# Optimization experiments

Hardware: AMD Instinct MI355X
Metric: run time of the kernel (lower is better)

## Reference

```python
import jax, jax.numpy as jnp
import numpy as np
from jax import lax

T_PN = (1, 1, 2, 2, 2, 4, 4, 4, 4, 4)
V_PN = (1, 2, 3, 4, 5, 6, 8, 10, 13, 16)
N_CODES = 16384
EMBED_DIM = 64
QRESI = 0.5           # abs(quant_resi), quant_resi = -0.5 -> ks=3 conv
K_SHARED = 4          # share_quant_resi


def _pool_mat(in_len, out_len):
    """torch F.interpolate(mode='area') == adaptive average pooling."""
    M = np.zeros((out_len, in_len), np.float32)
    for i in range(out_len):
        s = (i * in_len) // out_len
        e = -((-(i + 1) * in_len) // out_len)  # ceil((i+1)*in/out)
        M[i, s:e] = 1.0 / (e - s)
    return jnp.asarray(M)


def _lin_mat(in_len, out_len):
    """torch linear/trilinear upsample (align_corners=False) per-axis weights."""
    M = np.zeros((out_len, in_len), np.float32)
    if in_len == 1:
        M[:, 0] = 1.0
        return jnp.asarray(M)
    scale = in_len / out_len
    for i in range(out_len):
        src = max((i + 0.5) * scale - 0.5, 0.0)
        i0 = min(int(np.floor(src)), in_len - 1)
        i1 = min(i0 + 1, in_len - 1)
        w = src - i0
        M[i, i0] += 1.0 - w
        M[i, i1] += w
    return jnp.asarray(M)


def _resi_idx(si, n_scales):
    # ResConvAfterUpsampleList.__getitem__ : nearest tick to si/(n_scales-1)
    ticks = np.linspace(1.0 / 3 / K_SHARED, 1.0 - 1.0 / 3 / K_SHARED, K_SHARED)
    return int(np.argmin(np.abs(ticks - si / max(1, n_scales - 1))))


def _conv3d(x, w, b):
    y = lax.conv_general_dilated(x, w, (1, 1, 1), 'SAME',
                                 dimension_numbers=('NCDHW', 'OIDHW', 'NCDHW'))
    return y + b[None, :, None, None, None]


def setup_inputs() -> dict:
    key = jax.random.key(0)
    k1, k2, k3, k4 = jax.random.split(key, 4)
    z = jax.random.normal(k1, (8, EMBED_DIM, 4, 16, 16), dtype=jnp.float32)
    embeddings = jax.random.normal(k2, (N_CODES, EMBED_DIM), dtype=jnp.float32)
    Wq = jax.random.normal(k3, (K_SHARED, EMBED_DIM, EMBED_DIM, 3, 3, 3), dtype=jnp.float32) * 0.02
    bq = jax.random.normal(k4, (K_SHARED, EMBED_DIM), dtype=jnp.float32) * 0.02
    return {"z": z, "embeddings": embeddings, "Wq": Wq, "bq": bq}


def reference(z, embeddings, Wq, bq):
    B, C, T, H, W = z.shape
    S = len(V_PN)
    z_sg = lax.stop_gradient(z)
    accu = jnp.zeros_like(z)
    commit = jnp.asarray(0.0, z.dtype)
    ms_idx = []
    e_sq = jnp.sum(embeddings * embeddings, axis=1)  # [n_codes]
    for si, (tpn, pn) in enumerate(zip(T_PN, V_PN)):
        tpn = min(tpn, T)
        # rest uses detached accu (accu_h.data in torch)
        rest = z_sg - lax.stop_gradient(accu)
        if si != S - 1:
            rest = jnp.einsum('bcthw,ut,vh,xw->bcuvx', rest,
                              _pool_mat(T, tpn), _pool_mat(H, pn), _pool_mat(W, pn))
        zNC = rest.transpose(0, 2, 3, 4, 1).reshape(-1, C)  # [N, C]
        # ||z||^2 + ||e||^2 - 2 z.e  (the addmm)
        d = jnp.sum(zNC * zNC, axis=1, keepdims=True) + e_sq - 2.0 * (zNC @ embeddings.T)
        idx = jnp.argmin(d, axis=1).reshape(rest.shape[0], *rest.shape[2:])  # [B,t,p,p]
        ms_idx.append(idx)
        h = embeddings[idx].transpose(0, 4, 1, 2, 3)  # [B,C,t,p,p]
        if h.shape[2:] != (T, H, W):
            h = jnp.einsum('bcthw,ut,vh,xw->bcuvx', h,
                           _lin_mat(tpn, T), _lin_mat(pn, H), _lin_mat(pn, W))
        qi = _resi_idx(si, S)
        h = h * (1.0 - QRESI) + _conv3d(h, Wq[qi], bq[qi]) * QRESI
        accu = accu + h
        commit = commit + 0.25 * jnp.mean((accu - z_sg) ** 2)
    commit = commit / S
    emb_st = lax.stop_gradient(accu - z) + z  # straight-through
    # eval-mode stats come from the LAST scale's indices (loop-variable leak in torch)
    last = ms_idx[-1].reshape(-1)
    probs = jnp.bincount(last, length=N_CODES).astype(z.dtype) / last.shape[0]
    perplexity = jnp.exp(-jnp.sum(probs * jnp.log(probs + 1e-10)))
    usage = probs  # counts/total == calculate_batch_codebook_usage_percentage
    avg_usage = jnp.sum(usage > 1.0 / N_CODES).astype(z.dtype) / N_CODES
    return (emb_st, commit, perplexity, avg_usage, usage) + tuple(ms_idx)
```

## Files before the change

### kernel.cpp

```cpp
#include <hip/hip_runtime.h>
#include <math.h>


#define NCODES 16384
#define NELEM  524288
#define NSP    8192

#define RCH    8
#define RCODES (NCODES / RCH)

#define WS_ACCU   0ul
#define WS_HUP    4194304ul
#define WS_REST64 8388608ul
#define WS_PACC   8388608ul
#define WS_PART   12582912ul
#define WS_ZCL    16777216ul
#define WS_EHF    18874368ul
#define WS_ELF    20971520ul
#define WS_ESQ    23068672ul
#define WS_TWT    23134208ul
#define WS_IDX    24903680ul
#define WS_CNT    24936448ul
#define WS_FLAGL  25001984ul
#define WS_FLAGC  25034752ul
#define WS_SSE    25034816ul
#define WS_ENT    25034824ul
#define WS_USED   25034832ul
#define WS_RHF    25034848ul
#define WS_RLF    26083424ul

typedef __attribute__((ext_vector_type(8))) short short8;
typedef __attribute__((ext_vector_type(4))) float floatx4;

struct PBest { double d; int idx; int pad; };

__device__ __forceinline__ void gl2lds16(const void* g, void* l) {
  __builtin_amdgcn_global_load_lds(
      (const __attribute__((address_space(1))) unsigned int*)g,
      (__attribute__((address_space(3))) unsigned int*)l, 16, 0, 0);
}

__device__ inline short bf16rne(float f, float* hi) {
  unsigned u = __float_as_uint(f);
  unsigned r = (u + 0x7FFFu + ((u >> 16) & 1u)) >> 16;
  *hi = __uint_as_float(r << 16);
  return (short)r;
}

__global__ __launch_bounds__(256) void prep_kernel(
    const float* __restrict__ z, const float* __restrict__ emb, const float* __restrict__ Wq,
    double* __restrict__ accu, float* __restrict__ zcl,
    short* __restrict__ ehf, short* __restrict__ elf,
    float* __restrict__ esq, float* __restrict__ twt,
    int* __restrict__ counts, int* __restrict__ flagcnt,
    double* sse, double* ent, int* usedcnt)
{
  int i = blockIdx.x * 256 + threadIdx.x;
  if (i < NELEM) { accu[i] = 0.0; return; }
  i -= NELEM;
  if (i < NELEM) {
    int c = i & 63, w = (i >> 6) & 15, h = (i >> 10) & 15, t = (i >> 14) & 3, b = i >> 16;
    zcl[i] = z[(((b * 64 + c) * 4 + t) * 16 + h) * 16 + w];
    return;
  }
  i -= NELEM;
  if (i < NCODES * 64) {
    int j = i >> 6, c = i & 63;
    float v = emb[i];
    float hi; short h = bf16rne(v, &hi);
    float hi2; short l = bf16rne(v - hi, &hi2);
    int jt = j >> 4, nn = j & 15, hf = c >> 5, q = (c >> 3) & 3, ii = c & 7;
    size_t slot = ((size_t)(((jt * 2 + hf) * 64) + q * 16 + nn)) * 8 + ii;
    ehf[slot] = h; elf[slot] = l;
    return;
  }
  i -= NCODES * 64;
  if (i < NCODES) {
    float s = 0.f;
    for (int c = 0; c < 64; c++) { float v = emb[i * 64 + c]; s += v * v; }
    esq[i] = s; return;
  }
  i -= NCODES;
  if (i < 442368) {
    int qi = i / 110592; int r = i % 110592;
    int tap = r >> 12; int ci = (r >> 6) & 63; int co = r & 63;
    twt[i] = Wq[((qi * 64 + co) * 64 + ci) * 27 + tap];
    return;
  }
  i -= 442368;
  if (i < NCODES) { counts[i] = 0; return; }
  i -= NCODES;
  if (i < 16) {
    if (i < 10) flagcnt[i] = 0;
    else if (i == 10) *sse = 0.0;
    else if (i == 11) *ent = 0.0;
    else if (i == 12) *usedcnt = 0;
  }
}

__global__ __launch_bounds__(256) void pool_kernel(
    const float* __restrict__ zcl, const double* __restrict__ accu,
    double* __restrict__ rest64, short* __restrict__ rhf, short* __restrict__ rlf,
    int N, int tpn, int pn)
{
  __shared__ double psum[4][64];
  int n = blockIdx.x;
  int tid = threadIdx.x;
  int c = tid & 63, ck = tid >> 6;
  if (n >= N) {
    if (tid < 64) {
      int pt = n >> 4, m = n & 15, hf = tid >> 5, q = (tid >> 3) & 3, ii = tid & 7;
      size_t slot = ((size_t)(((pt * 2 + hf) * 64) + q * 16 + m)) * 8 + ii;
      rhf[slot] = 0; rlf[slot] = 0;
    }
    return;
  }
  int ppn = pn * pn;
  int b = n / (tpn * ppn); int r = n % (tpn * ppn);
  int u = r / ppn; r %= ppn; int v = r / pn; int x = r % pn;
  int t0 = (u * 4) / tpn, t1 = ((u + 1) * 4 + tpn - 1) / tpn;
  int h0 = (v * 16) / pn, h1 = ((v + 1) * 16 + pn - 1) / pn;
  int w0 = (x * 16) / pn, w1 = ((x + 1) * 16 + pn - 1) / pn;
  int nt = t1 - t0, nh = h1 - h0, nw = w1 - w0;
  int M = nt * nh * nw;
  int chunk = (M + 3) >> 2;
  int m0 = ck * chunk; int m1 = m0 + chunk; if (m1 > M) m1 = M;
  double s = 0.0;
  if (m0 < m1) {
    int tmp = m0 / nw; int wi = m0 - tmp * nw;
    int ti = tmp / nh; int hi = tmp - ti * nh;
    for (int m = m0; m < m1; m++) {
      size_t off = (size_t)((((b * 4 + t0 + ti) * 16 + h0 + hi) * 16 + w0 + wi) * 64 + c);
      s += (double)zcl[off] - accu[off];
      if (++wi == nw) { wi = 0; if (++hi == nh) { hi = 0; ++ti; } }
    }
  }
  psum[ck][c] = s;
  __syncthreads();
  if (tid < 64) {
    double t = ((psum[0][c] + psum[1][c]) + psum[2][c]) + psum[3][c];
    float wt = 1.f / (float)nt, wh = 1.f / (float)nh, ww = 1.f / (float)nw;
    double rv = t * (double)wt * (double)wh * (double)ww;
    rest64[(size_t)n * 64 + c] = rv;
    float rv32 = (float)rv;
    float hi; short h = bf16rne(rv32, &hi);
    float hi2; short l = bf16rne(rv32 - hi, &hi2);
    int pt = n >> 4, m = n & 15, hf = c >> 5, q = (c >> 3) & 3, ii = c & 7;
    size_t slot = ((size_t)(((pt * 2 + hf) * 64) + q * 16 + m)) * 8 + ii;
    rhf[slot] = h; rlf[slot] = l;
  }
}

__global__ __launch_bounds__(256) void pool_part_kernel(
    const float* __restrict__ zcl, const double* __restrict__ accu,
    double* __restrict__ ppool, int N, int tpn, int pn, int SPL)
{
  __shared__ double psum[4][64];
  int n = blockIdx.x;
  int sp = blockIdx.y;
  int tid = threadIdx.x;
  int c = tid & 63, ck = tid >> 6;
  int ppn = pn * pn;
  int b = n / (tpn * ppn); int r = n % (tpn * ppn);
  int u = r / ppn; r %= ppn; int v = r / pn; int x = r % pn;
  int t0 = (u * 4) / tpn, t1 = ((u + 1) * 4 + tpn - 1) / tpn;
  int h0 = (v * 16) / pn, h1 = ((v + 1) * 16 + pn - 1) / pn;
  int w0 = (x * 16) / pn, w1 = ((x + 1) * 16 + pn - 1) / pn;
  int nt = t1 - t0, nh = h1 - h0, nw = w1 - w0;
  int M = nt * nh * nw;
  int C = SPL * 4;
  int chunk = (M + C - 1) / C;
  int m0 = (sp * 4 + ck) * chunk; int m1 = m0 + chunk;
  if (m0 > M) m0 = M;
  if (m1 > M) m1 = M;
  double s = 0.0;
  if (m0 < m1) {
    int tmp = m0 / nw; int wi = m0 - tmp * nw;
    int ti = tmp / nh; int hi = tmp - ti * nh;
    for (int m = m0; m < m1; m++) {
      size_t off = (size_t)((((b * 4 + t0 + ti) * 16 + h0 + hi) * 16 + w0 + wi) * 64 + c);
      s += (double)zcl[off] - accu[off];
      if (++wi == nw) { wi = 0; if (++hi == nh) { hi = 0; ++ti; } }
    }
  }
  psum[ck][c] = s;
  __syncthreads();
  if (tid < 64) {
    double t = ((psum[0][c] + psum[1][c]) + psum[2][c]) + psum[3][c];
    ppool[((size_t)n * SPL + sp) * 64 + c] = t;
  }
}

__global__ __launch_bounds__(256) void pool_finish_kernel(
    const double* __restrict__ ppool, double* __restrict__ rest64,
    short* __restrict__ rhf, short* __restrict__ rlf,
    int N, int tpn, int pn, int SPL)
{
  __shared__ double psum[4][64];
  int n = blockIdx.x;
  int tid = threadIdx.x;
  int c = tid & 63, ck = tid >> 6;
  if (n >= N) {
    if (tid < 64) {
      int pt = n >> 4, m = n & 15, hf = tid >> 5, q = (tid >> 3) & 3, ii = tid & 7;
      size_t slot = ((size_t)(((pt * 2 + hf) * 64) + q * 16 + m)) * 8 + ii;
      rhf[slot] = 0; rlf[slot] = 0;
    }
    return;
  }
  int ppn = pn * pn;
  int b = n / (tpn * ppn); int r = n % (tpn * ppn);
  int u = r / ppn; r %= ppn; int v = r / pn; int x = r % pn;
  int t0 = (u * 4) / tpn, t1 = ((u + 1) * 4 + tpn - 1) / tpn;
  int h0 = (v * 16) / pn, h1 = ((v + 1) * 16 + pn - 1) / pn;
  int w0 = (x * 16) / pn, w1 = ((x + 1) * 16 + pn - 1) / pn;
  int nt = t1 - t0, nh = h1 - h0, nw = w1 - w0;
  (void)b; (void)t0; (void)h0; (void)w0;
  int q4 = SPL >> 2;
  const double* pp = ppool + ((size_t)n * SPL) * 64 + c;
  double s = 0.0;
  for (int sp = ck * q4; sp < (ck + 1) * q4; sp++) s += pp[(size_t)sp * 64];
  psum[ck][c] = s;
  __syncthreads();
  if (tid < 64) {
    double t = ((psum[0][c] + psum[1][c]) + psum[2][c]) + psum[3][c];
    float wt = 1.f / (float)nt, wh = 1.f / (float)nh, ww = 1.f / (float)nw;
    double rv = t * (double)wt * (double)wh * (double)ww;
    rest64[(size_t)n * 64 + c] = rv;
    float rv32 = (float)rv;
    float hi; short h = bf16rne(rv32, &hi);
    float hi2; short l = bf16rne(rv32 - hi, &hi2);
    int pt = n >> 4, m = n & 15, hf = c >> 5, qq = (c >> 3) & 3, ii = c & 7;
    size_t slot = ((size_t)(((pt * 2 + hf) * 64) + qq * 16 + m)) * 8 + ii;
    rhf[slot] = h; rlf[slot] = l;
  }
}

__global__ __launch_bounds__(256) void argmin_kernel(
    const short* __restrict__ rhf, const short* __restrict__ rlf,
    const short* __restrict__ ehf, const short* __restrict__ elf,
    const float* __restrict__ esq, float4* __restrict__ part,
    int NSpad, int nstripes)
{
  __shared__ short8 Bh[8][2][64];
  __shared__ short8 Bl[8][2][64];
  __shared__ float esql[128];
  int tid = threadIdx.x;
  int pbase = blockIdx.x * 64;
  int ch = blockIdx.y;
  int wv64 = tid & ~63, ln = tid & 63;
  int w = tid >> 6, lane = tid & 63, col = lane & 15;
  const short8* sAH = (const short8*)(rhf + (size_t)pbase * 64);
  const short8* sAL = (const short8*)(rlf + (size_t)pbase * 64);
  short8 ah0 = sAH[(2 * w + 0) * 64 + lane], ah1 = sAH[(2 * w + 1) * 64 + lane];
  short8 al0 = sAL[(2 * w + 0) * 64 + lane], al1 = sAL[(2 * w + 1) * 64 + lane];
  float M1[4], M2[4]; int I1[4];
#pragma unroll
  for (int r = 0; r < 4; r++) { M1[r] = -3.4e38f; M2[r] = -3.4e38f; I1[r] = 0x7fffffff; }
  for (int s = 0; s < nstripes; s++) {
    int j0 = ch * (nstripes * 128) + s * 128;
    __syncthreads();
    {
      const short8* sH = (const short8*)(ehf + (size_t)j0 * 64);
      const short8* sL = (const short8*)(elf + (size_t)j0 * 64);
      short8* dH = (short8*)Bh; short8* dL = (short8*)Bl;
#pragma unroll
      for (int it = 0; it < 4; it++) {
        int idx = it * 256 + wv64;
        gl2lds16(sH + idx + ln, dH + idx);
        gl2lds16(sL + idx + ln, dL + idx);
      }
      if (tid < 128) esql[tid] = esq[j0 + tid];
    }
    __syncthreads();
    floatx4 acc[8];
#pragma unroll
    for (int jt = 0; jt < 8; jt++) {
      float c0 = -0.5f * esql[jt * 16 + col];
      acc[jt] = (floatx4){c0, c0, c0, c0};
    }
#pragma unroll
    for (int jt = 0; jt < 8; jt++) {
      short8 bh0 = Bh[jt][0][lane], bl0 = Bl[jt][0][lane];
      short8 bh1 = Bh[jt][1][lane], bl1 = Bl[jt][1][lane];
      acc[jt] = __builtin_amdgcn_mfma_f32_16x16x32_bf16(al0, bh0, acc[jt], 0, 0, 0);
      acc[jt] = __builtin_amdgcn_mfma_f32_16x16x32_bf16(ah0, bl0, acc[jt], 0, 0, 0);
      acc[jt] = __builtin_amdgcn_mfma_f32_16x16x32_bf16(ah0, bh0, acc[jt], 0, 0, 0);
      acc[jt] = __builtin_amdgcn_mfma_f32_16x16x32_bf16(al1, bh1, acc[jt], 0, 0, 0);
      acc[jt] = __builtin_amdgcn_mfma_f32_16x16x32_bf16(ah1, bl1, acc[jt], 0, 0, 0);
      acc[jt] = __builtin_amdgcn_mfma_f32_16x16x32_bf16(ah1, bh1, acc[jt], 0, 0, 0);
    }
#pragma unroll
    for (int jt = 0; jt < 8; jt++) {
      int j = j0 + jt * 16 + col;
#pragma unroll
      for (int r = 0; r < 4; r++) {
        float a = acc[jt][r];
        bool c = a > M1[r];
        M2[r] = __builtin_amdgcn_fmed3f(a, M1[r], M2[r]);
        M1[r] = fmaxf(a, M1[r]);
        I1[r] = c ? j : I1[r];
      }
    }
  }
#pragma unroll
  for (int off = 1; off < 16; off <<= 1) {
#pragma unroll
    for (int r = 0; r < 4; r++) {
      float o1 = __shfl_xor(M1[r], off);
      int   oi = __shfl_xor(I1[r], off);
      float o2 = __shfl_xor(M2[r], off);
      bool bwin = (o1 > M1[r]) || (o1 == M1[r] && oi < I1[r]);
      float nm2 = bwin ? fmaxf(M1[r], o2) : fmaxf(M2[r], o1);
      if (bwin) { M1[r] = o1; I1[r] = oi; }
      M2[r] = nm2;
    }
  }
  if (col == 0) {
    int quad = lane >> 4;
#pragma unroll
    for (int r = 0; r < 4; r++) {
      int p = pbase + w * 16 + quad * 4 + r;
      part[(size_t)ch * NSpad + p] =
          make_float4(-2.f * M1[r], -2.f * M2[r], __int_as_float(I1[r]), 0.f);
    }
  }
}

__global__ __launch_bounds__(256) void reduce_kernel(
    const float4* __restrict__ part, int* __restrict__ idx_cur,
    float* __restrict__ out_idx, int* flagcnt, int* flaglist,
    int N, int NSpad, int nch)
{
  int n = blockIdx.x * 256 + threadIdx.x;
  if (n >= N) return;
  float m1 = 3.4e38f, m2 = 3.4e38f; int i1 = 0x7fffffff;
  for (int ch = 0; ch < nch; ch++) {
    float4 q = part[(size_t)ch * NSpad + n];
    float o1 = q.x, o2 = q.y; int oi = __float_as_int(q.z);
    bool bwin = (o1 < m1) || (o1 == m1 && oi < i1);
    float nm2 = bwin ? fminf(m1, o2) : fminf(m2, o1);
    if (bwin) { m1 = o1; i1 = oi; }
    m2 = nm2;
  }
  idx_cur[n] = i1;
  out_idx[n] = (float)i1;
  if (m2 - m1 < 0.01f) {
    int pos = atomicAdd(flagcnt, 1);
    flaglist[pos] = n;
  }
}

__global__ __launch_bounds__(256) void refine_kernel(
    const double* __restrict__ rest64, const float* __restrict__ emb,
    const int* __restrict__ flagcnt, const int* __restrict__ flaglist,
    PBest* __restrict__ pbest)
{
  __shared__ double bmS[4];
  __shared__ int    biS[4];
  int cnt = *flagcnt;
  int ch = blockIdx.y;
  int tid = threadIdx.x;
  int lane = tid & 63, wv = tid >> 6;
  int c4 = lane & 15;
  int g = tid >> 4;
  for (int f = blockIdx.x; f < cnt; f += 1024) {
    int n = flaglist[f];
    const double* rp = rest64 + (size_t)n * 64 + c4 * 4;
    double r0 = rp[0], r1 = rp[1], r2 = rp[2], r3 = rp[3];
    double best = 1e300; int bidx = 0x7fffffff;
    int jb0 = ch * RCODES + g * 128;
#pragma unroll 1
    for (int s16 = 0; s16 < 8; s16++) {
      int jb = jb0 + s16 * 16;
      double a[16];
#pragma unroll
      for (int m = 0; m < 16; m++) {
        float4 ev = *(const float4*)&emb[(size_t)(jb + m) * 64 + c4 * 4];
        double d0 = r0 - (double)ev.x, d1 = r1 - (double)ev.y;
        double d2 = r2 - (double)ev.z, d3 = r3 - (double)ev.w;
        a[m] = (d0 * d0 + d1 * d1) + (d2 * d2 + d3 * d3);
      }
#pragma unroll
      for (int p = 0; p < 4; p++) {
        int s = 1 << p;
        int bit = (lane >> p) & 1;
        int half = 8 >> p;
#pragma unroll
        for (int k = 0; k < half; k++) {
          double lo = a[2 * k], hi = a[2 * k + 1];
          double send = bit ? lo : hi;
          double keep = bit ? hi : lo;
          a[k] = keep + __shfl_xor(send, s);
        }
      }
      double tot = a[0];
      int j = jb + c4;
      if (tot < best) { best = tot; bidx = j; }
    }
#pragma unroll
    for (int off = 1; off < 64; off <<= 1) {
      double ob = __shfl_xor(best, off);
      int    oi = __shfl_xor(bidx, off);
      if (ob < best || (ob == best && oi < bidx)) { best = ob; bidx = oi; }
    }
    if (lane == 0) { bmS[wv] = best; biS[wv] = bidx; }
    __syncthreads();
    if (tid == 0) {
      double b = bmS[0]; int bi2 = biS[0];
      for (int w2 = 1; w2 < 4; w2++) {
        double ob = bmS[w2]; int oi = biS[w2];
        if (ob < b || (ob == b && oi < bi2)) { b = ob; bi2 = oi; }
      }
      pbest[f * RCH + ch].d = b; pbest[f * RCH + ch].idx = bi2;
    }
    __syncthreads();
  }
}

__global__ __launch_bounds__(256) void refine_merge_kernel(
    const PBest* __restrict__ pbest, const int* __restrict__ flagcnt,
    const int* __restrict__ flaglist, int* __restrict__ idx_cur,
    float* __restrict__ out_idx)
{
  int f = blockIdx.x * 256 + threadIdx.x;
  if (f >= *flagcnt) return;
  double best = 1e300; int bidx = 0x7fffffff;
  for (int ch = 0; ch < RCH; ch++) {
    double d = pbest[f * RCH + ch].d; int j = pbest[f * RCH + ch].idx;
    if (d < best || (d == best && j < bidx)) { best = d; bidx = j; }
  }
  int n = flaglist[f];
  idx_cur[n] = bidx;
  out_idx[n] = (float)bidx;
}

__device__ inline void axis_map(int L, int outlen, int i, int* j0, int* j1, float* a0, float* a1) {
  if (L == 1) { *j0 = 0; *j1 = 0; *a0 = 1.f; *a1 = 0.f; return; }
  double scale = (double)L / (double)outlen;
  double src = (i + 0.5) * scale - 0.5;
  if (src < 0.0) src = 0.0;
  int i0 = (int)floor(src); if (i0 > L - 1) i0 = L - 1;
  int i1 = i0 + 1; if (i1 > L - 1) i1 = L - 1;
  double wv = src - (double)i0;
  if (i0 == i1) {
    float p = (float)(1.0 - wv), q = (float)wv;
    *a0 = p + q; *a1 = 0.f;
  } else { *a0 = (float)(1.0 - wv); *a1 = (float)wv; }
  *j0 = i0; *j1 = i1;
}

__global__ __launch_bounds__(256) void upsample_kernel(
    const float* __restrict__ emb, const int* __restrict__ idx_cur,
    float* __restrict__ hup, int tpn, int pn)
{
  int e = blockIdx.x * 256 + threadIdx.x;
  int c = e & 63, w = (e >> 6) & 15, h = (e >> 10) & 15, t = (e >> 14) & 3, b = e >> 16;
  int t0, t1, h0, h1, w0, w1; float ta0, ta1, ha0, ha1, wa0, wa1;
  axis_map(tpn, 4, t, &t0, &t1, &ta0, &ta1);
  axis_map(pn, 16, h, &h0, &h1, &ha0, &ha1);
  axis_map(pn, 16, w, &w0, &w1, &wa0, &wa1);
  int ti[2] = {t0, t1}; float ta[2] = {ta0, ta1};
  int hi[2] = {h0, h1}; float ha[2] = {ha0, ha1};
  int wi[2] = {w0, w1}; float wa[2] = {wa0, wa1};
  double val = 0.0;
  for (int a = 0; a < 2; a++)
    for (int bb = 0; bb < 2; bb++)
      for (int cc = 0; cc < 2; cc++) {
        double wgt = (double)ta[a] * (double)ha[bb] * (double)wa[cc];
        if (wgt != 0.0) {
          int code = idx_cur[((b * tpn + ti[a]) * pn + hi[bb]) * pn + wi[cc]];
          val += wgt * (double)emb[(size_t)code * 64 + c];
        }
      }
  hup[e] = (float)val;
}

#define WLV   864
#define WLPAD (WLV * 4 + 128)
__global__ __launch_bounds__(256) void conv_part_kernel(
    const float* __restrict__ hup, const float* __restrict__ twt,
    float* __restrict__ pacc, int qi)
{
  __shared__ float hl[2][4][3][6][18];
  __shared__ __align__(16) float wl[2][WLPAD];
  int bid = blockIdx.x;
  int coH = bid & 1, s2 = (bid >> 1) & 1, hq = (bid >> 2) & 3, t = (bid >> 4) & 3, b = bid >> 6;
  int tid = threadIdx.x;
  int c4 = tid & 15;
  int wq = (tid >> 4) & 3;
  int th = tid >> 6;
  int h = hq * 4 + th, w0 = wq * 4;
  int wv64 = tid & ~63, ln = tid & 63;

  int lofs[6]; int gofs[6]; bool pred[6];
#pragma unroll
  for (int j = 0; j < 6; j++) {
    int i = tid + j * 256;
    bool vs = i < 1296;
    int ii = vs ? i : 0;
    int cc = ii & 3; int jj = ii >> 2;
    int ww = jj % 18; int k = jj / 18;
    int hh = k % 6, tt = k / 6;
    int gt = t - 1 + tt, gh = hq * 4 - 1 + hh, gw = ww - 1;
    bool inb = gt >= 0 && gt < 4 && gh >= 0 && gh < 16 && gw >= 0 && gw < 16;
    lofs[j] = ((cc * 3 + tt) * 6 + hh) * 18 + ww;
    gofs[j] = inb ? ((((b * 4 + gt) * 16 + gh) * 16 + gw) * 64 + cc) : 0;
    pred[j] = vs && inb;
  }
  float* hlf0 = &hl[0][0][0][0][0];
  float* hlf1 = &hl[1][0][0][0][0];

#define STAGE_W(bb, ci0v)                                                      \
  {                                                                            \
    const float4* srcb = (const float4*)twt;                                   \
    float4* dstb = (float4*)wl[bb];                                            \
    _Pragma("unroll")                                                          \
    for (int k2 = 0; k2 < 4; k2++) {                                           \
      int idx = k2 * 256 + wv64;                                               \
      if (idx < WLV) {                                                         \
        int i2 = idx + ln; if (i2 > WLV - 1) i2 = WLV - 1;                     \
        int f4 = i2 & 7; int tc = i2 >> 3;                                     \
        int tap = tc >> 2, cc2 = tc & 3;                                       \
        const float4* g = srcb + ((size_t)((qi * 27 + tap) * 64 + (ci0v) + cc2) * 16 + coH * 8 + f4); \
        gl2lds16(g, dstb + idx);                                               \
      }                                                                        \
    }                                                                          \
  }

  float acc[4][2];
#pragma unroll
  for (int wi = 0; wi < 4; wi++) { acc[wi][0] = 0.f; acc[wi][1] = 0.f; }

  {
    int ci0 = s2 * 32;
    float hreg[6];
#pragma unroll
    for (int j = 0; j < 6; j++) hreg[j] = pred[j] ? hup[gofs[j] + ci0] : 0.f;
    STAGE_W(0, ci0);
#pragma unroll
    for (int j = 0; j < 6; j++)
      if (tid + j * 256 < 1296) hlf0[lofs[j]] = hreg[j];
    __syncthreads();
  }

  int cur = 0;
#pragma unroll 1
  for (int c4i = 0; c4i < 8; c4i++) {
    int nxt = cur ^ 1;
    float hreg[6];
    if (c4i < 7) {
      int ci0n = s2 * 32 + (c4i + 1) * 4;
#pragma unroll
      for (int j = 0; j < 6; j++) hreg[j] = pred[j] ? hup[gofs[j] + ci0n] : 0.f;
      STAGE_W(nxt, ci0n);
    }
    const float* wlc = wl[cur];
#pragma unroll 1
    for (int dtdh = 0; dtdh < 9; dtdh++) {
      int dt = dtdh / 3, dh = dtdh % 3;
#pragma unroll
      for (int cc = 0; cc < 4; cc++) {
        float hv[6];
#pragma unroll
        for (int k = 0; k < 6; k++) hv[k] = hl[cur][cc][dt][th + dh][w0 + k];
#pragma unroll
        for (int dw = 0; dw < 3; dw++) {
          float2 wf = *(const float2*)&wlc[(((dtdh * 3 + dw) * 4 + cc) << 5) + c4 * 2];
#pragma unroll
          for (int wi = 0; wi < 4; wi++) {
            float hvv = hv[wi + dw];
            acc[wi][0] += hvv * wf.x; acc[wi][1] += hvv * wf.y;
          }
        }
      }
    }
    if (c4i < 7) {
      float* hlfn = nxt ? hlf1 : hlf0;
#pragma unroll
      for (int j = 0; j < 6; j++)
        if (tid + j * 256 < 1296) hlfn[lofs[j]] = hreg[j];
    }
    __syncthreads();
    cur = nxt;
  }
#undef STAGE_W

  float* base = &pacc[(size_t)s2 * NELEM +
                      (size_t)((((b * 4 + t) * 16 + h) * 16 + w0) * 64 + coH * 32 + c4 * 2)];
#pragma unroll
  for (int wi = 0; wi < 4; wi++) {
    float2 v = make_float2(acc[wi][0], acc[wi][1]);
    *(float2*)(base + wi * 64) = v;
  }
}

__global__ __launch_bounds__(256) void conv_combine_kernel(
    const float* __restrict__ pacc, const float* __restrict__ hup,
    const float* __restrict__ bq, const float* __restrict__ zcl,
    double* __restrict__ accu, double* sse, int qi)
{
  __shared__ double red[256];
  int tid = threadIdx.x;
  int e = blockIdx.x * 256 + tid;
  int co = e & 63;
  double cv = ((double)pacc[e] + (double)pacc[(size_t)NELEM + e]) + (double)bq[qi * 64 + co];
  double hu = (double)hup[e];
  double na = accu[e] + 0.5 * hu + 0.5 * cv;
  accu[e] = na;
  double df = na - (double)zcl[e];
  red[tid] = df * df;
  __syncthreads();
  for (int s = 128; s > 0; s >>= 1) { if (tid < s) red[tid] += red[tid + s]; __syncthreads(); }
  if (tid == 0) atomicAdd(sse, red[0]);
}

__global__ __launch_bounds__(256) void bincount_kernel(const int* __restrict__ idx_cur, int* counts) {
  int i = blockIdx.x * 256 + threadIdx.x;
  if (i < NSP) atomicAdd(&counts[idx_cur[i]], 1);
}

__global__ __launch_bounds__(256) void stats_kernel(
    const int* __restrict__ counts, float* __restrict__ usage_out, double* ent, int* usedcnt)
{
  __shared__ double re[256];
  __shared__ int ru[256];
  int j = blockIdx.x * 256 + threadIdx.x;
  int cnt = counts[j];
  double p = (double)cnt / 8192.0;
  usage_out[j] = (float)p;
  re[threadIdx.x] = p * log(p + 1e-10);
  ru[threadIdx.x] = cnt > 0 ? 1 : 0;
  __syncthreads();
  for (int s = 128; s > 0; s >>= 1) {
    if (threadIdx.x < s) { re[threadIdx.x] += re[threadIdx.x + s]; ru[threadIdx.x] += ru[threadIdx.x + s]; }
    __syncthreads();
  }
  if (threadIdx.x == 0) { atomicAdd(ent, re[0]); atomicAdd(usedcnt, ru[0]); }
}

__global__ void final_kernel(const double* sse, const double* ent, const int* usedcnt, float* out) {
  if (threadIdx.x == 0) {
    out[NELEM]     = (float)(*sse * 0.25 / 524288.0 / 10.0);
    out[NELEM + 1] = (float)exp(-*ent);
    out[NELEM + 2] = (float)((double)*usedcnt / 16384.0);
  }
}

__global__ __launch_bounds__(256) void embst_kernel(const double* __restrict__ accu, float* __restrict__ out) {
  int e = blockIdx.x * 256 + threadIdx.x;
  int w = e & 15, h = (e >> 4) & 15, t = (e >> 8) & 3, c = (e >> 10) & 63, b = e >> 16;
  out[e] = (float)accu[(size_t)(((((b * 4 + t) * 16 + h) * 16 + w) * 64) + c)];
}

extern "C" void kernel_launch(void* const* d_in, const int* in_sizes, int n_in,
                              void* d_out, int out_size, void* d_ws, size_t ws_size,
                              hipStream_t stream) {
  static const int T_PN_h[10] = {1, 1, 2, 2, 2, 4, 4, 4, 4, 4};
  static const int V_PN_h[10] = {1, 2, 3, 4, 5, 6, 8, 10, 13, 16};
  static const int QI_h[10]   = {0, 0, 1, 1, 1, 2, 2, 3, 3, 3};
  static const int NS_h[10]   = {8, 32, 144, 256, 400, 1152, 2048, 3200, 5408, 8192};
  static const int OB_h[10]   = {540675, 540683, 540715, 540859, 541115,
                                 541515, 542667, 544715, 547915, 553323};
  static const int NCH_h[10]  = {128, 128, 64, 64, 64, 32, 32, 32, 16, 16};
  static const int SPL_h[10]  = {128, 32, 8, 4, 4, 1, 1, 1, 1, 1};

  const float* z   = (const float*)d_in[0];
  const float* emb = (const float*)d_in[1];
  const float* Wq  = (const float*)d_in[2];
  const float* bq  = (const float*)d_in[3];
  float* out = (float*)d_out;
  char* ws = (char*)d_ws;

  double* accu    = (double*)(ws + WS_ACCU);
  float*  hup     = (float*)(ws + WS_HUP);
  double* rest64  = (double*)(ws + WS_REST64);
  float*  pacc    = (float*)(ws + WS_PACC);
  float4* part    = (float4*)(ws + WS_PART);
  PBest*  pbest   = (PBest*)(ws + WS_PART);
  double* ppool   = (double*)(ws + WS_PART);
  float*  zcl     = (float*)(ws + WS_ZCL);
  short*  ehf     = (short*)(ws + WS_EHF);
  short*  elf     = (short*)(ws + WS_ELF);
  float*  esq     = (float*)(ws + WS_ESQ);
  float*  twt     = (float*)(ws + WS_TWT);
  int*    idx_cur = (int*)(ws + WS_IDX);
  int*    counts  = (int*)(ws + WS_CNT);
  int*    flaglist= (int*)(ws + WS_FLAGL);
  int*    flagcnt = (int*)(ws + WS_FLAGC);
  double* sse     = (double*)(ws + WS_SSE);
  double* ent     = (double*)(ws + WS_ENT);
  int*    usedcnt = (int*)(ws + WS_USED);
  short*  rhf     = (short*)(ws + WS_RHF);
  short*  rlf     = (short*)(ws + WS_RLF);

  prep_kernel<<<10049, 256, 0, stream>>>(z, emb, Wq, accu, zcl, ehf, elf, esq, twt,
                                         counts, flagcnt, sse, ent, usedcnt);

  for (int si = 0; si < 10; si++) {
    int tpn = T_PN_h[si], pn = V_PN_h[si], N = NS_h[si];
    int NSpad = (N + 63) & ~63;
    int nch = NCH_h[si];
    int nstripes = (NCODES / nch) / 128;
    int SPL = SPL_h[si];
    if (SPL > 1) {
      dim3 pg(N, SPL);
      pool_part_kernel<<<pg, 256, 0, stream>>>(zcl, accu, ppool, N, tpn, pn, SPL);
      pool_finish_kernel<<<NSpad, 256, 0, stream>>>(ppool, rest64, rhf, rlf, N, tpn, pn, SPL);
    } else {
      pool_kernel<<<NSpad, 256, 0, stream>>>(zcl, accu, rest64, rhf, rlf, N, tpn, pn);
    }
    dim3 ag(NSpad / 64, nch);
    argmin_kernel<<<ag, 256, 0, stream>>>(rhf, rlf, ehf, elf, esq, part, NSpad, nstripes);
    reduce_kernel<<<(N + 255) / 256, 256, 0, stream>>>(part, idx_cur, out + OB_h[si],
                                                       flagcnt + si, flaglist, N, NSpad, nch);
    dim3 rg(1024, RCH);
    refine_kernel<<<rg, 256, 0, stream>>>(rest64, emb, flagcnt + si, flaglist, pbest);
    refine_merge_kernel<<<(N + 255) / 256, 256, 0, stream>>>(pbest, flagcnt + si, flaglist,
                                                             idx_cur, out + OB_h[si]);
    upsample_kernel<<<NELEM / 256, 256, 0, stream>>>(emb, idx_cur, hup, tpn, pn);
    conv_part_kernel<<<512, 256, 0, stream>>>(hup, twt, pacc, QI_h[si]);
    conv_combine_kernel<<<NELEM / 256, 256, 0, stream>>>(pacc, hup, bq, zcl, accu, sse, QI_h[si]);
  }

  bincount_kernel<<<32, 256, 0, stream>>>(idx_cur, counts);
  stats_kernel<<<64, 256, 0, stream>>>(counts, out + 524291, ent, usedcnt);
  final_kernel<<<1, 64, 0, stream>>>(sse, ent, usedcnt, out);
  embst_kernel<<<NELEM / 256, 256, 0, stream>>>(accu, out);
}
```

Before: 1.662 ms.

## Drop low-part residual MFMA terms and widen refine margin with error bound

Removes the al*bh MFMA products from the bf16-split distance GEMM, cutting matrix work per tile from six MFMAs to four. To keep the argmin exact, the pool kernels now compute the squared norm of the residual low part per row, and a new kernel computes the maximum codebook squared norm. The reduce kernel widens the margin for flagging ambiguous rows by a Cauchy-Schwarz bound built from these two values, so more rows may go to the fp64 refine pass. The argmin chunk count for the first two scales also drops from 128 to 64.

```diff
diff --git a/kernel.cpp b/kernel.cpp
--- a/kernel.cpp
+++ b/kernel.cpp
@@ -28,6 +28,8 @@
 #define WS_USED   25034832ul
 #define WS_RHF    25034848ul
 #define WS_RLF    26083424ul
+#define WS_ANM    27132000ul
+#define WS_EMX    27164768ul
 
 typedef __attribute__((ext_vector_type(8))) short short8;
 typedef __attribute__((ext_vector_type(4))) float floatx4;
@@ -98,10 +100,26 @@
   }
 }
 
+__global__ __launch_bounds__(256) void emax_kernel(
+    const float* __restrict__ esq, float* __restrict__ emx)
+{
+  __shared__ float red[256];
+  int tid = threadIdx.x;
+  float m = 0.f;
+  for (int j = tid; j < NCODES; j += 256) m = fmaxf(m, esq[j]);
+  red[tid] = m;
+  __syncthreads();
+  for (int s = 128; s > 0; s >>= 1) {
+    if (tid < s) red[tid] = fmaxf(red[tid], red[tid + s]);
+    __syncthreads();
+  }
+  if (tid == 0) *emx = red[0];
+}
+
 __global__ __launch_bounds__(256) void pool_kernel(
     const float* __restrict__ zcl, const double* __restrict__ accu,
     double* __restrict__ rest64, short* __restrict__ rhf, short* __restrict__ rlf,
-    int N, int tpn, int pn)
+    float* __restrict__ alnorm, int N, int tpn, int pn)
 {
   __shared__ double psum[4][64];
   int n = blockIdx.x;
@@ -148,6 +166,11 @@
     int pt = n >> 4, m = n & 15, hf = c >> 5, q = (c >> 3) & 3, ii = c & 7;
     size_t slot = ((size_t)(((pt * 2 + hf) * 64) + q * 16 + m)) * 8 + ii;
     rhf[slot] = h; rlf[slot] = l;
+    float alv = rv32 - hi;
+    float a2 = alv * alv;
+#pragma unroll
+    for (int off = 1; off < 64; off <<= 1) a2 += __shfl_xor(a2, off);
+    if (c == 0) alnorm[n] = a2;
   }
 }
 
@@ -194,7 +217,7 @@
 __global__ __launch_bounds__(256) void pool_finish_kernel(
     const double* __restrict__ ppool, double* __restrict__ rest64,
     short* __restrict__ rhf, short* __restrict__ rlf,
-    int N, int tpn, int pn, int SPL)
+    float* __restrict__ alnorm, int N, int tpn, int pn, int SPL)
 {
   __shared__ double psum[4][64];
   int n = blockIdx.x;
@@ -233,11 +256,16 @@
     int pt = n >> 4, m = n & 15, hf = c >> 5, qq = (c >> 3) & 3, ii = c & 7;
     size_t slot = ((size_t)(((pt * 2 + hf) * 64) + qq * 16 + m)) * 8 + ii;
     rhf[slot] = h; rlf[slot] = l;
+    float alv = rv32 - hi;
+    float a2 = alv * alv;
+#pragma unroll
+    for (int off = 1; off < 64; off <<= 1) a2 += __shfl_xor(a2, off);
+    if (c == 0) alnorm[n] = a2;
   }
 }
 
 __global__ __launch_bounds__(256) void argmin_kernel(
-    const short* __restrict__ rhf, const short* __restrict__ rlf,
+    const short* __restrict__ rhf,
     const short* __restrict__ ehf, const short* __restrict__ elf,
     const float* __restrict__ esq, float4* __restrict__ part,
     int NSpad, int nstripes)
@@ -251,9 +279,7 @@
   int wv64 = tid & ~63, ln = tid & 63;
   int w = tid >> 6, lane = tid & 63, col = lane & 15;
   const short8* sAH = (const short8*)(rhf + (size_t)pbase * 64);
-  const short8* sAL = (const short8*)(rlf + (size_t)pbase * 64);
   short8 ah0 = sAH[(2 * w + 0) * 64 + lane], ah1 = sAH[(2 * w + 1) * 64 + lane];
-  short8 al0 = sAL[(2 * w + 0) * 64 + lane], al1 = sAL[(2 * w + 1) * 64 + lane];
   float M1[4], M2[4]; int I1[4];
 #pragma unroll
   for (int r = 0; r < 4; r++) { M1[r] = -3.4e38f; M2[r] = -3.4e38f; I1[r] = 0x7fffffff; }
@@ -283,10 +309,8 @@
     for (int jt = 0; jt < 8; jt++) {
       short8 bh0 = Bh[jt][0][lane], bl0 = Bl[jt][0][lane];
       short8 bh1 = Bh[jt][1][lane], bl1 = Bl[jt][1][lane];
-      acc[jt] = __builtin_amdgcn_mfma_f32_16x16x32_bf16(al0, bh0, acc[jt], 0, 0, 0);
       acc[jt] = __builtin_amdgcn_mfma_f32_16x16x32_bf16(ah0, bl0, acc[jt], 0, 0, 0);
       acc[jt] = __builtin_amdgcn_mfma_f32_16x16x32_bf16(ah0, bh0, acc[jt], 0, 0, 0);
-      acc[jt] = __builtin_amdgcn_mfma_f32_16x16x32_bf16(al1, bh1, acc[jt], 0, 0, 0);
       acc[jt] = __builtin_amdgcn_mfma_f32_16x16x32_bf16(ah1, bl1, acc[jt], 0, 0, 0);
       acc[jt] = __builtin_amdgcn_mfma_f32_16x16x32_bf16(ah1, bh1, acc[jt], 0, 0, 0);
     }
@@ -328,7 +352,8 @@
 }
 
 __global__ __launch_bounds__(256) void reduce_kernel(
-    const float4* __restrict__ part, int* __restrict__ idx_cur,
+    const float4* __restrict__ part, const float* __restrict__ alnorm,
+    const float* __restrict__ emx, int* __restrict__ idx_cur,
     float* __restrict__ out_idx, int* flagcnt, int* flaglist,
     int N, int NSpad, int nch)
 {
@@ -345,7 +370,8 @@
   }
   idx_cur[n] = i1;
   out_idx[n] = (float)i1;
-  if (m2 - m1 < 0.01f) {
+  float margin = 0.01f + 4.0f * sqrtf(alnorm[n] * (*emx));
+  if (m2 - m1 < margin) {
     int pos = atomicAdd(flagcnt, 1);
     flaglist[pos] = n;
   }
@@ -662,7 +688,7 @@
   static const int NS_h[10]   = {8, 32, 144, 256, 400, 1152, 2048, 3200, 5408, 8192};
   static const int OB_h[10]   = {540675, 540683, 540715, 540859, 541115,
                                  541515, 542667, 544715, 547915, 553323};
-  static const int NCH_h[10]  = {128, 128, 64, 64, 64, 32, 32, 32, 16, 16};
+  static const int NCH_h[10]  = {64, 64, 64, 64, 64, 32, 32, 32, 16, 16};
   static const int SPL_h[10]  = {128, 32, 8, 4, 4, 1, 1, 1, 1, 1};
 
   const float* z   = (const float*)d_in[0];
@@ -693,9 +719,12 @@
   int*    usedcnt = (int*)(ws + WS_USED);
   short*  rhf     = (short*)(ws + WS_RHF);
   short*  rlf     = (short*)(ws + WS_RLF);
+  float*  alnorm  = (float*)(ws + WS_ANM);
+  float*  emx     = (float*)(ws + WS_EMX);
 
   prep_kernel<<<10049, 256, 0, stream>>>(z, emb, Wq, accu, zcl, ehf, elf, esq, twt,
                                          counts, flagcnt, sse, ent, usedcnt);
+  emax_kernel<<<1, 256, 0, stream>>>(esq, emx);
 
   for (int si = 0; si < 10; si++) {
     int tpn = T_PN_h[si], pn = V_PN_h[si], N = NS_h[si];
@@ -706,13 +735,15 @@
     if (SPL > 1) {
       dim3 pg(N, SPL);
       pool_part_kernel<<<pg, 256, 0, stream>>>(zcl, accu, ppool, N, tpn, pn, SPL);
-      pool_finish_kernel<<<NSpad, 256, 0, stream>>>(ppool, rest64, rhf, rlf, N, tpn, pn, SPL);
+      pool_finish_kernel<<<NSpad, 256, 0, stream>>>(ppool, rest64, rhf, rlf, alnorm,
+                                                    N, tpn, pn, SPL);
     } else {
-      pool_kernel<<<NSpad, 256, 0, stream>>>(zcl, accu, rest64, rhf, rlf, N, tpn, pn);
+      pool_kernel<<<NSpad, 256, 0, stream>>>(zcl, accu, rest64, rhf, rlf, alnorm, N, tpn, pn);
     }
     dim3 ag(NSpad / 64, nch);
-    argmin_kernel<<<ag, 256, 0, stream>>>(rhf, rlf, ehf, elf, esq, part, NSpad, nstripes);
-    reduce_kernel<<<(N + 255) / 256, 256, 0, stream>>>(part, idx_cur, out + OB_h[si],
+    argmin_kernel<<<ag, 256, 0, stream>>>(rhf, ehf, elf, esq, part, NSpad, nstripes);
+    reduce_kernel<<<(N + 255) / 256, 256, 0, stream>>>(part, alnorm, emx, idx_cur,
+                                                       out + OB_h[si],
                                                        flagcnt + si, flaglist, N, NSpad, nch);
     dim3 rg(1024, RCH);
     refine_kernel<<<rg, 256, 0, stream>>>(rest64, emb, flagcnt + si, flaglist, pbest);
```

New measurement: 2.173 ms. 30.8% more time.
